# Kernel tuning notes

Measured on AMD Instinct MI355X. Metric: run time of the kernel, lower is better.

The kernel has to match this reference:

```python
import jax, jax.numpy as jnp
import numpy as np

F_IN, F_OUT, N_HEADS = 64, 256, 4
HEAD_DIM = F_OUT // N_HEADS


def setup_inputs() -> dict:
    key = jax.random.key(0)
    ks = jax.random.split(key, 9)
    s_in = 1.0 / np.sqrt(F_IN)
    s_out = 1.0 / np.sqrt(F_OUT)
    return {
        "x": jax.random.normal(ks[0], (4, 32, F_IN, 512), dtype=jnp.float32),
        "Wq": jax.random.normal(ks[1], (F_IN, F_OUT), dtype=jnp.float32) * s_in,
        "bq": jax.random.normal(ks[2], (F_OUT,), dtype=jnp.float32) * 0.01,
        "Wk": jax.random.normal(ks[3], (F_IN, F_OUT), dtype=jnp.float32) * s_in,
        "bk": jax.random.normal(ks[4], (F_OUT,), dtype=jnp.float32) * 0.01,
        "Wv": jax.random.normal(ks[5], (F_IN, F_OUT), dtype=jnp.float32) * s_in,
        "bv": jax.random.normal(ks[6], (F_OUT,), dtype=jnp.float32) * 0.01,
        "Wo": jax.random.normal(ks[7], (F_OUT, F_OUT), dtype=jnp.float32) * s_out,
        "bo": jax.random.normal(ks[8], (F_OUT,), dtype=jnp.float32) * 0.01,
    }


def reference(x, Wq, bq, Wk, bk, Wv, bv, Wo, bo):
    B, N, Fdim, T = x.shape
    xp = jnp.transpose(x, (0, 1, 3, 2))  # [B, N, T, F]
    q = xp @ Wq + bq  # [B, N, T, f_out]
    k = xp @ Wk + bk
    v = xp @ Wv + bv
    # split f_out into heads: [B, N, T, H, hd]
    q = q.reshape(B, N, T, N_HEADS, HEAD_DIM)
    k = k.reshape(B, N, T, N_HEADS, HEAD_DIM)
    v = v.reshape(B, N, T, N_HEADS, HEAD_DIM)
    scale = 1.0 / np.sqrt(HEAD_DIM)
    # full TxT score matrix per (batch, node, head), as in the original
    scores = jnp.einsum("bnqhd,bnkhd->bnhqk", q, k) * scale
    attn = jax.nn.softmax(scores, axis=-1)
    out = jnp.einsum("bnhqk,bnkhd->bnqhd", attn, v)  # [B, N, T, H, hd]
    out = out.reshape(B, N, T, F_OUT)  # head-concat along feature dim
    out = out @ Wo + bo  # fc_out; dropout is identity at inference
    return jnp.transpose(out, (0, 1, 3, 2))  # [B, N, f_out, T]
```

## Files before the change

kernel.cpp:

```cpp
#include <hip/hip_runtime.h>

constexpr int kT = 512;
constexpr int kF = 64;
constexpr int kC = 256;
constexpr int kH = 4;
constexpr int kHD = 64;
constexpr int kBN = 128;

typedef __attribute__((ext_vector_type(4))) float f32x4;
typedef __attribute__((ext_vector_type(8))) short s16x8;
typedef __attribute__((ext_vector_type(4))) unsigned int u32x4;

__device__ inline unsigned short f2bf(float f) {
  unsigned int u = __float_as_uint(f);
  u += 0x7fff + ((u >> 16) & 1);
  return (unsigned short)(u >> 16);
}

__device__ inline float max3f(float a, float b, float c) {
  return fmaxf(fmaxf(a, b), c);
}

__device__ inline float exp2_hw(float x) {
  float r;
  asm("v_exp_f32 %0, %1" : "=v"(r) : "v"(x));
  return r;
}

__global__ __launch_bounds__(256) void k_prep(
    const float* __restrict__ Wq, const float* __restrict__ Wk,
    const float* __restrict__ Wv, const float* __restrict__ Wo,
    unsigned short* __restrict__ WB, unsigned short* __restrict__ WoT) {
  int i = blockIdx.x * 256 + threadIdx.x;
  const int total = 768 * 64 + 256 * 256;
  for (; i < total; i += gridDim.x * 256) {
    if (i < 768 * 64) {
      int c = i >> 6, f = i & 63;
      int arr = c >> 8, cc = c & 255;
      const float* W = (arr == 0) ? Wq : (arr == 1) ? Wk : Wv;
      WB[i] = f2bf(W[f * 256 + cc]);
    } else {
      int j = i - 768 * 64;
      int co = j >> 8, c = j & 255;
      WoT[j] = f2bf(Wo[c * 256 + co]);
    }
  }
}

__global__ __launch_bounds__(1024, 4) void k_fattn(
    const float* __restrict__ x, const unsigned short* __restrict__ WB,
    const float* __restrict__ bq, const float* __restrict__ bk,
    const float* __restrict__ bv, unsigned short* __restrict__ Aw) {
  __shared__ __align__(16) unsigned char smem[149504];
  unsigned char* Kl = smem;
  unsigned char* VtB = smem + 65536;
  unsigned short* xC = (unsigned short*)(smem + 131072);

  const int tid = threadIdx.x;
  const int lbn = blockIdx.x >> 2;
  const int h = blockIdx.x & 3;
  const int lane = tid & 63, wid = tid >> 6;
  const int lr = lane & 15, lg = lane >> 4;
  const int swz = (lr & 7) << 4;

  const float kQscale = 0.180336880111120426f;
  const unsigned short* WBq = WB + (size_t)(h * 64) * 64;
  const unsigned short* WBk = WB + (size_t)(256 + h * 64) * 64;
  const unsigned short* WBv = WB + (size_t)(512 + h * 64) * 64;

  s16x8 qf[2][2];

  for (int tch = 0; tch < 4; ++tch) {
    __syncthreads();
    const float* xb = x + (size_t)lbn * kF * kT + tch * 128;
#pragma unroll
    for (int it = 0; it < 2; ++it) {
      int idx = tid + it * 1024;
      int f = idx >> 5, t4 = idx & 31;
      float4 v = *(const float4*)(xb + f * kT + t4 * 4);
      xC[(t4 * 4 + 0) * 72 + f] = f2bf(v.x);
      xC[(t4 * 4 + 1) * 72 + f] = f2bf(v.y);
      xC[(t4 * 4 + 2) * 72 + f] = f2bf(v.z);
      xC[(t4 * 4 + 3) * 72 + f] = f2bf(v.w);
    }
    __syncthreads();

#pragma unroll
    for (int j = 0; j < 4; ++j) {
      const int tau = wid * 4 + j;
      const int isV = tau >> 5;
      const int tl = tau & 31;
      const int ct = tl >> 3, tt = tl & 7;
      const unsigned short* Wsrc = isV ? WBv : WBk;
      s16x8 af0 = *(const s16x8*)(Wsrc + (ct * 16 + lr) * 64 + lg * 8);
      s16x8 af1 = *(const s16x8*)(Wsrc + (ct * 16 + lr) * 64 + 32 + lg * 8);
      s16x8 bf0 = *(const s16x8*)&xC[(tt * 16 + lr) * 72 + lg * 8];
      s16x8 bf1 = *(const s16x8*)&xC[(tt * 16 + lr) * 72 + 32 + lg * 8];
      if (!isV) {
        f32x4 a = {0.f, 0.f, 0.f, 0.f};
        a = __builtin_amdgcn_mfma_f32_16x16x32_bf16(af0, bf0, a, 0, 0, 0);
        a = __builtin_amdgcn_mfma_f32_16x16x32_bf16(af1, bf1, a, 0, 0, 0);
        const int dbase = ct * 16 + lg * 4;
        const int t = tch * 128 + tt * 16 + lr;
        float v0 = a[0] + bk[h * 64 + dbase + 0];
        float v1 = a[1] + bk[h * 64 + dbase + 1];
        float v2 = a[2] + bk[h * 64 + dbase + 2];
        float v3 = a[3] + bk[h * 64 + dbase + 3];
        unsigned long long pk =
            (unsigned long long)f2bf(v0) |
            ((unsigned long long)f2bf(v1) << 16) |
            ((unsigned long long)f2bf(v2) << 32) |
            ((unsigned long long)f2bf(v3) << 48);
        *(unsigned long long*)(Kl + ((t * 128 + dbase * 2) ^ ((t & 7) << 4))) = pk;
      } else {
        f32x4 a = {0.f, 0.f, 0.f, 0.f};
        a = __builtin_amdgcn_mfma_f32_16x16x32_bf16(bf0, af0, a, 0, 0, 0);
        a = __builtin_amdgcn_mfma_f32_16x16x32_bf16(bf1, af1, a, 0, 0, 0);
        const int d = ct * 16 + lr;
        const float bias = bv[h * 64 + d];
        const int t0 = tch * 128 + tt * 16 + lg * 4;
        const int pos0 = ((t0 >> 5) << 5) | (((t0 >> 2) & 3) << 3) |
                         (((t0 >> 4) & 1) << 2);
        unsigned long long pk =
            (unsigned long long)f2bf(a[0] + bias) |
            ((unsigned long long)f2bf(a[1] + bias) << 16) |
            ((unsigned long long)f2bf(a[2] + bias) << 32) |
            ((unsigned long long)f2bf(a[3] + bias) << 48);
        *(unsigned long long*)(VtB + ((d * 1024 + pos0 * 2) ^ ((d & 7) << 4))) = pk;
      }
    }

    if ((wid >> 2) == tch) {
      f32x4 qa[2][4];
#pragma unroll
      for (int qt = 0; qt < 2; ++qt) {
        const int ttq = (wid & 3) * 2 + qt;
#pragma unroll
        for (int ct = 0; ct < 4; ++ct) {
          s16x8 af0 = *(const s16x8*)(WBq + (ct * 16 + lr) * 64 + lg * 8);
          s16x8 af1 = *(const s16x8*)(WBq + (ct * 16 + lr) * 64 + 32 + lg * 8);
          s16x8 bf0 = *(const s16x8*)&xC[(ttq * 16 + lr) * 72 + lg * 8];
          s16x8 bf1 = *(const s16x8*)&xC[(ttq * 16 + lr) * 72 + 32 + lg * 8];
          f32x4 a = {0.f, 0.f, 0.f, 0.f};
          a = __builtin_amdgcn_mfma_f32_16x16x32_bf16(af0, bf0, a, 0, 0, 0);
          a = __builtin_amdgcn_mfma_f32_16x16x32_bf16(af1, bf1, a, 0, 0, 0);
          const int dbase = ct * 16 + lg * 4;
#pragma unroll
          for (int r = 0; r < 4; ++r)
            a[r] = (a[r] + bq[h * 64 + dbase + r]) * kQscale;
          qa[qt][ct] = a;
        }
      }
      const int sel = lg >> 1;
#pragma unroll
      for (int qt = 0; qt < 2; ++qt)
#pragma unroll
        for (int half = 0; half < 2; ++half) {
          unsigned int w[4];
#pragma unroll
          for (int i2 = 0; i2 < 4; ++i2) {
            const int r0 = (i2 & 1) * 2;
            const int lgp = (lg & 1) * 2 + (i2 >> 1);
            const int src = lgp * 16 + lr;
            float loA = __shfl(qa[qt][half * 2 + 0][r0], src);
            float hiA = __shfl(qa[qt][half * 2 + 1][r0], src);
            float loB = __shfl(qa[qt][half * 2 + 0][r0 + 1], src);
            float hiB = __shfl(qa[qt][half * 2 + 1][r0 + 1], src);
            float eA = sel ? hiA : loA;
            float eB = sel ? hiB : loB;
            asm("v_cvt_pk_bf16_f32 %0, %1, %2"
                : "=v"(w[i2]) : "v"(eA), "v"(eB));
          }
          qf[qt][half] =
              __builtin_bit_cast(s16x8, (u32x4){w[0], w[1], w[2], w[3]});
        }
    }
  }
  __syncthreads();

  unsigned short* Ab = Aw + (size_t)lbn * kT * kC + h * kHD;
  const int qbase = wid * 32;

  f32x4 o0[4] = {{0,0,0,0},{0,0,0,0},{0,0,0,0},{0,0,0,0}};
  f32x4 o1[4] = {{0,0,0,0},{0,0,0,0},{0,0,0,0},{0,0,0,0}};
  float m0 = -3e38f, m1 = -3e38f, l0 = 0.f, l1 = 0.f;

  const int koff = (lg * 16) ^ swz;
  const unsigned char* kp0 = Kl + lr * 128 + koff;
  const unsigned char* kp1 = Kl + lr * 128 + (koff ^ 64);
  const unsigned char* vp0 = VtB + lr * 1024 + ((lg * 16) ^ swz);
  const unsigned char* vp1 = VtB + lr * 1024 + (((lg * 16) ^ 64) ^ swz);

  unsigned int w0[8], w1[8];

#define SOFTMAX_QT(sa, m, l, o, w)                                            \
  {                                                                           \
    float g0 = max3f(sa[0][0], sa[0][1], sa[0][2]);                           \
    float g1 = max3f(sa[0][3], sa[1][0], sa[1][1]);                           \
    float g2 = max3f(sa[1][2], sa[1][3], sa[2][0]);                           \
    float g3 = max3f(sa[2][1], sa[2][2], sa[2][3]);                           \
    float g4 = max3f(sa[3][0], sa[3][1], sa[3][2]);                           \
    float tm = fmaxf(max3f(g0, g1, g2), max3f(g3, g4, sa[3][3]));             \
    if (__any(tm > m + 8.0f)) {                                               \
      tm = fmaxf(tm, __shfl_xor(tm, 16));                                     \
      tm = fmaxf(tm, __shfl_xor(tm, 32));                                     \
      float mn = fmaxf(m, tm);                                                \
      float al = exp2_hw(m - mn);                                             \
      m = mn;                                                                 \
      l *= al;                                                                \
      float aq0 = __shfl(al, (lane & 48) | (lg * 4 + 0));                     \
      float aq1 = __shfl(al, (lane & 48) | (lg * 4 + 1));                     \
      float aq2 = __shfl(al, (lane & 48) | (lg * 4 + 2));                     \
      float aq3 = __shfl(al, (lane & 48) | (lg * 4 + 3));                     \
      _Pragma("unroll")                                                       \
      for (int dt = 0; dt < 4; ++dt) {                                        \
        o[dt][0] *= aq0; o[dt][1] *= aq1;                                     \
        o[dt][2] *= aq2; o[dt][3] *= aq3;                                     \
      }                                                                       \
    }                                                                         \
    _Pragma("unroll")                                                         \
    for (int s = 0; s < 4; ++s) {                                             \
      float e0 = exp2_hw(sa[s][0] - m);                                       \
      float e1 = exp2_hw(sa[s][1] - m);                                       \
      float e2 = exp2_hw(sa[s][2] - m);                                       \
      float e3 = exp2_hw(sa[s][3] - m);                                       \
      l += (e0 + e1) + (e2 + e3);                                             \
      asm("v_cvt_pk_bf16_f32 %0, %1, %2" : "=v"(w[2*s]) : "v"(e0), "v"(e1));  \
      asm("v_cvt_pk_bf16_f32 %0, %1, %2" : "=v"(w[2*s+1]) : "v"(e2), "v"(e3));\
    }                                                                         \
  }

  for (int kc = 0; kc < 8; ++kc) {
    f32x4 sa0[4], sa1[4];
#pragma unroll
    for (int s = 0; s < 4; ++s) {
      s16x8 kf0 = *(const s16x8*)(kp0 + s * 2048);
      s16x8 kf1 = *(const s16x8*)(kp1 + s * 2048);
      f32x4 z0 = {0.f, 0.f, 0.f, 0.f};
      z0 = __builtin_amdgcn_mfma_f32_16x16x32_bf16(kf0, qf[0][0], z0, 0, 0, 0);
      z0 = __builtin_amdgcn_mfma_f32_16x16x32_bf16(kf1, qf[0][1], z0, 0, 0, 0);
      sa0[s] = z0;
      f32x4 z1 = {0.f, 0.f, 0.f, 0.f};
      z1 = __builtin_amdgcn_mfma_f32_16x16x32_bf16(kf0, qf[1][0], z1, 0, 0, 0);
      z1 = __builtin_amdgcn_mfma_f32_16x16x32_bf16(kf1, qf[1][1], z1, 0, 0, 0);
      sa1[s] = z1;
    }
    kp0 += 8192;
    kp1 += 8192;

    SOFTMAX_QT(sa0, m0, l0, o0, w0)
    SOFTMAX_QT(sa1, m1, l1, o1, w1)

    s16x8 pa00 = __builtin_bit_cast(s16x8, (u32x4){w0[0], w0[1], w0[2], w0[3]});
    s16x8 pa01 = __builtin_bit_cast(s16x8, (u32x4){w0[4], w0[5], w0[6], w0[7]});
    s16x8 pa10 = __builtin_bit_cast(s16x8, (u32x4){w1[0], w1[1], w1[2], w1[3]});
    s16x8 pa11 = __builtin_bit_cast(s16x8, (u32x4){w1[4], w1[5], w1[6], w1[7]});

#pragma unroll
    for (int dt = 0; dt < 4; ++dt) {
      s16x8 vb = *(const s16x8*)(vp0 + dt * 16384);
      o0[dt] = __builtin_amdgcn_mfma_f32_16x16x32_bf16(pa00, vb, o0[dt], 0, 0, 0);
      o1[dt] = __builtin_amdgcn_mfma_f32_16x16x32_bf16(pa10, vb, o1[dt], 0, 0, 0);
    }
#pragma unroll
    for (int dt = 0; dt < 4; ++dt) {
      s16x8 vb = *(const s16x8*)(vp1 + dt * 16384);
      o0[dt] = __builtin_amdgcn_mfma_f32_16x16x32_bf16(pa01, vb, o0[dt], 0, 0, 0);
      o1[dt] = __builtin_amdgcn_mfma_f32_16x16x32_bf16(pa11, vb, o1[dt], 0, 0, 0);
    }
    vp0 += 128;
    vp1 += 128;
  }
#undef SOFTMAX_QT

#pragma unroll
  for (int qt = 0; qt < 2; ++qt) {
    float l = (qt == 0) ? l0 : l1;
    f32x4* o = (qt == 0) ? o0 : o1;
    float l2 = l + __shfl_xor(l, 16);
    float lr4 = l2 + __shfl_xor(l2, 32);
    float li0 = 1.0f / __shfl(lr4, (lane & 48) | (lg * 4 + 0));
    float li1 = 1.0f / __shfl(lr4, (lane & 48) | (lg * 4 + 1));
    float li2 = 1.0f / __shfl(lr4, (lane & 48) | (lg * 4 + 2));
    float li3 = 1.0f / __shfl(lr4, (lane & 48) | (lg * 4 + 3));
    const int qb = qbase + qt * 16;
#pragma unroll
    for (int r = 0; r < 4; ++r) {
      float li = (r == 0) ? li0 : (r == 1) ? li1 : (r == 2) ? li2 : li3;
      unsigned short* orow = Ab + (size_t)(qb + lg * 4 + r) * kC;
#pragma unroll
      for (int dt = 0; dt < 4; ++dt)
        orow[dt * 16 + lr] = f2bf(o[dt][r] * li);
    }
  }
}

__global__ __launch_bounds__(512) void k_proj(
    const unsigned short* __restrict__ Aw, const unsigned short* __restrict__ WoT,
    const float* __restrict__ bo, float* __restrict__ out) {
  __shared__ __align__(16) unsigned char Al[128 * 512];

  const int tid = threadIdx.x;
  const int lbn = blockIdx.x >> 2;
  const int tch = blockIdx.x & 3;
  const int t0 = tch * 128;

  const uint4* Asrc = (const uint4*)(Aw + ((size_t)lbn * kT + t0) * kC);
#pragma unroll
  for (int i = 0; i < 8; ++i) {
    int idx = tid + i * 512;
    int trow = idx >> 5, cc = idx & 31;
    *(uint4*)(Al + ((trow * 512 + cc * 16) ^ ((trow & 7) << 4))) = Asrc[idx];
  }
  __syncthreads();

  const int lane = tid & 63, wid = tid >> 6;
  const int lr = lane & 15, lg = lane >> 4;
  const int swz = (lr & 7) << 4;
  const int tb = (wid >> 2) * 64;
  const int cob = (wid & 3) * 64;

  float* ob = out + (size_t)lbn * kC * kT;

  for (int ci = 0; ci < 4; ++ci) {
    const int co0 = cob + ci * 16;
    s16x8 af[8];
#pragma unroll
    for (int kc = 0; kc < 8; ++kc)
      af[kc] = *(const s16x8*)(WoT + (size_t)(co0 + lr) * 256 + kc * 32 + lg * 8);
    float b4[4];
#pragma unroll
    for (int r = 0; r < 4; ++r) b4[r] = bo[co0 + lg * 4 + r];

#pragma unroll
    for (int tj = 0; tj < 4; ++tj) {
      const unsigned char* ap = Al + (tb + tj * 16 + lr) * 512;
      f32x4 acc = {0.f, 0.f, 0.f, 0.f};
#pragma unroll
      for (int kc = 0; kc < 8; ++kc) {
        s16x8 bfr = *(const s16x8*)(ap + ((kc * 64 + lg * 16) ^ swz));
        acc = __builtin_amdgcn_mfma_f32_16x16x32_bf16(af[kc], bfr, acc, 0, 0, 0);
      }
      int t = t0 + tb + tj * 16 + lr;
#pragma unroll
      for (int r = 0; r < 4; ++r)
        ob[(size_t)(co0 + lg * 4 + r) * kT + t] = acc[r] + b4[r];
    }
  }
}

extern "C" void kernel_launch(void* const* d_in, const int* in_sizes, int n_in,
                              void* d_out, int out_size, void* d_ws, size_t ws_size,
                              hipStream_t stream) {
  const float* x  = (const float*)d_in[0];
  const float* Wq = (const float*)d_in[1];
  const float* bq = (const float*)d_in[2];
  const float* Wk = (const float*)d_in[3];
  const float* bk = (const float*)d_in[4];
  const float* Wv = (const float*)d_in[5];
  const float* bv = (const float*)d_in[6];
  const float* Wo = (const float*)d_in[7];
  const float* bo = (const float*)d_in[8];
  float* out = (float*)d_out;

  const size_t wElems = 768 * 64 + 256 * 256;
  const size_t aBytes = (size_t)kBN * kT * kC * 2;
  if (ws_size < wElems * 2 + aBytes) return;

  unsigned short* WB  = (unsigned short*)d_ws;
  unsigned short* WoT = WB + 768 * 64;
  unsigned short* A   = WB + wElems;

  k_prep<<<dim3(448), dim3(256), 0, stream>>>(Wq, Wk, Wv, Wo, WB, WoT);
  k_fattn<<<dim3(kBN * kH), dim3(1024), 0, stream>>>(x, WB, bq, bk, bv, A);
  k_proj<<<dim3(kBN * 4), dim3(512), 0, stream>>>(A, WoT, bo, out);
}
```

Before: 118.4 us.

## Swizzle x staging tile, remap block order, prefetch V fragments, use packed bf16 converts

The x staging buffer in LDS gets an XOR swizzle (144-byte rows) in place of the padded 72-element layout, to cut bank conflicts on fragment reads. Block IDs are remapped so consecutive blocks spread across node/head groups, which changes how work lands on XCDs and caches. V fragments are loaded before the softmax so LDS latency overlaps the exp work. Manual bf16 rounding is replaced with the hardware v_cvt_pk_bf16_f32 instruction throughout. The early V loads raise register pressure in a 1024-thread block, and the block remap may hurt L2 locality of x reuse.

Result: no change. 120.7 us (+1.9%).

```diff
diff --git a/kernel.cpp b/kernel.cpp
--- a/kernel.cpp
+++ b/kernel.cpp
@@ -15,6 +15,12 @@
   unsigned int u = __float_as_uint(f);
   u += 0x7fff + ((u >> 16) & 1);
   return (unsigned short)(u >> 16);
+}
+
+__device__ inline unsigned int cvt_pk(float a, float b) {
+  unsigned int w;
+  asm("v_cvt_pk_bf16_f32 %0, %1, %2" : "=v"(w) : "v"(a), "v"(b));
+  return w;
 }
 
 __device__ inline float max3f(float a, float b, float c) {
@@ -54,11 +60,13 @@
   __shared__ __align__(16) unsigned char smem[149504];
   unsigned char* Kl = smem;
   unsigned char* VtB = smem + 65536;
-  unsigned short* xC = (unsigned short*)(smem + 131072);
+  unsigned char* xCb = smem + 131072;
 
   const int tid = threadIdx.x;
-  const int lbn = blockIdx.x >> 2;
-  const int h = blockIdx.x & 3;
+  const int bid = blockIdx.x;
+  const int orig = (bid & 7) * 64 + (bid >> 3);
+  const int lbn = orig >> 2;
+  const int h = orig & 3;
   const int lane = tid & 63, wid = tid >> 6;
   const int lr = lane & 15, lg = lane >> 4;
   const int swz = (lr & 7) << 4;
@@ -68,6 +76,9 @@
   const unsigned short* WBk = WB + (size_t)(256 + h * 64) * 64;
   const unsigned short* WBv = WB + (size_t)(512 + h * 64) * 64;
 
+#define XFRAG(r, c) (const s16x8*)(xCb + (r) * 144 + \
+    (((c) * 2) ^ ((((r) >> 2) & 7) << 4)))
+
   s16x8 qf[2][2];
 
   for (int tch = 0; tch < 4; ++tch) {
@@ -78,10 +89,15 @@
       int idx = tid + it * 1024;
       int f = idx >> 5, t4 = idx & 31;
       float4 v = *(const float4*)(xb + f * kT + t4 * 4);
-      xC[(t4 * 4 + 0) * 72 + f] = f2bf(v.x);
-      xC[(t4 * 4 + 1) * 72 + f] = f2bf(v.y);
-      xC[(t4 * 4 + 2) * 72 + f] = f2bf(v.z);
-      xC[(t4 * 4 + 3) * 72 + f] = f2bf(v.w);
+      unsigned int wlo = cvt_pk(v.x, v.y);
+      unsigned int whi = cvt_pk(v.z, v.w);
+      const int fb = f * 2;
+      const int colb = (fb & 15) | ((((fb >> 4) ^ (t4 & 7))) << 4);
+      unsigned char* rp = xCb + (t4 * 4) * 144 + colb;
+      *(unsigned short*)(rp + 0 * 144) = (unsigned short)wlo;
+      *(unsigned short*)(rp + 1 * 144) = (unsigned short)(wlo >> 16);
+      *(unsigned short*)(rp + 2 * 144) = (unsigned short)whi;
+      *(unsigned short*)(rp + 3 * 144) = (unsigned short)(whi >> 16);
     }
     __syncthreads();
 
@@ -94,24 +110,20 @@
       const unsigned short* Wsrc = isV ? WBv : WBk;
       s16x8 af0 = *(const s16x8*)(Wsrc + (ct * 16 + lr) * 64 + lg * 8);
       s16x8 af1 = *(const s16x8*)(Wsrc + (ct * 16 + lr) * 64 + 32 + lg * 8);
-      s16x8 bf0 = *(const s16x8*)&xC[(tt * 16 + lr) * 72 + lg * 8];
-      s16x8 bf1 = *(const s16x8*)&xC[(tt * 16 + lr) * 72 + 32 + lg * 8];
+      s16x8 bf0 = *XFRAG(tt * 16 + lr, lg * 8);
+      s16x8 bf1 = *XFRAG(tt * 16 + lr, 32 + lg * 8);
       if (!isV) {
         f32x4 a = {0.f, 0.f, 0.f, 0.f};
         a = __builtin_amdgcn_mfma_f32_16x16x32_bf16(af0, bf0, a, 0, 0, 0);
         a = __builtin_amdgcn_mfma_f32_16x16x32_bf16(af1, bf1, a, 0, 0, 0);
         const int dbase = ct * 16 + lg * 4;
         const int t = tch * 128 + tt * 16 + lr;
-        float v0 = a[0] + bk[h * 64 + dbase + 0];
-        float v1 = a[1] + bk[h * 64 + dbase + 1];
-        float v2 = a[2] + bk[h * 64 + dbase + 2];
-        float v3 = a[3] + bk[h * 64 + dbase + 3];
-        unsigned long long pk =
-            (unsigned long long)f2bf(v0) |
-            ((unsigned long long)f2bf(v1) << 16) |
-            ((unsigned long long)f2bf(v2) << 32) |
-            ((unsigned long long)f2bf(v3) << 48);
-        *(unsigned long long*)(Kl + ((t * 128 + dbase * 2) ^ ((t & 7) << 4))) = pk;
+        uint2 pk;
+        pk.x = cvt_pk(a[0] + bk[h * 64 + dbase + 0],
+                      a[1] + bk[h * 64 + dbase + 1]);
+        pk.y = cvt_pk(a[2] + bk[h * 64 + dbase + 2],
+                      a[3] + bk[h * 64 + dbase + 3]);
+        *(uint2*)(Kl + ((t * 128 + dbase * 2) ^ ((t & 7) << 4))) = pk;
       } else {
         f32x4 a = {0.f, 0.f, 0.f, 0.f};
         a = __builtin_amdgcn_mfma_f32_16x16x32_bf16(bf0, af0, a, 0, 0, 0);
@@ -121,12 +133,10 @@
         const int t0 = tch * 128 + tt * 16 + lg * 4;
         const int pos0 = ((t0 >> 5) << 5) | (((t0 >> 2) & 3) << 3) |
                          (((t0 >> 4) & 1) << 2);
-        unsigned long long pk =
-            (unsigned long long)f2bf(a[0] + bias) |
-            ((unsigned long long)f2bf(a[1] + bias) << 16) |
-            ((unsigned long long)f2bf(a[2] + bias) << 32) |
-            ((unsigned long long)f2bf(a[3] + bias) << 48);
-        *(unsigned long long*)(VtB + ((d * 1024 + pos0 * 2) ^ ((d & 7) << 4))) = pk;
+        uint2 pk;
+        pk.x = cvt_pk(a[0] + bias, a[1] + bias);
+        pk.y = cvt_pk(a[2] + bias, a[3] + bias);
+        *(uint2*)(VtB + ((d * 1024 + pos0 * 2) ^ ((d & 7) << 4))) = pk;
       }
     }
 
@@ -139,8 +149,8 @@
         for (int ct = 0; ct < 4; ++ct) {
           s16x8 af0 = *(const s16x8*)(WBq + (ct * 16 + lr) * 64 + lg * 8);
           s16x8 af1 = *(const s16x8*)(WBq + (ct * 16 + lr) * 64 + 32 + lg * 8);
-          s16x8 bf0 = *(const s16x8*)&xC[(ttq * 16 + lr) * 72 + lg * 8];
-          s16x8 bf1 = *(const s16x8*)&xC[(ttq * 16 + lr) * 72 + 32 + lg * 8];
+          s16x8 bf0 = *XFRAG(ttq * 16 + lr, lg * 8);
+          s16x8 bf1 = *XFRAG(ttq * 16 + lr, 32 + lg * 8);
           f32x4 a = {0.f, 0.f, 0.f, 0.f};
           a = __builtin_amdgcn_mfma_f32_16x16x32_bf16(af0, bf0, a, 0, 0, 0);
           a = __builtin_amdgcn_mfma_f32_16x16x32_bf16(af1, bf1, a, 0, 0, 0);
@@ -166,10 +176,7 @@
             float hiA = __shfl(qa[qt][half * 2 + 1][r0], src);
             float loB = __shfl(qa[qt][half * 2 + 0][r0 + 1], src);
             float hiB = __shfl(qa[qt][half * 2 + 1][r0 + 1], src);
-            float eA = sel ? hiA : loA;
-            float eB = sel ? hiB : loB;
-            asm("v_cvt_pk_bf16_f32 %0, %1, %2"
-                : "=v"(w[i2]) : "v"(eA), "v"(eB));
+            w[i2] = cvt_pk(sel ? hiA : loA, sel ? hiB : loB);
           }
           qf[qt][half] =
               __builtin_bit_cast(s16x8, (u32x4){w[0], w[1], w[2], w[3]});
@@ -177,6 +184,7 @@
     }
   }
   __syncthreads();
+#undef XFRAG
 
   unsigned short* Ab = Aw + (size_t)lbn * kT * kC + h * kHD;
   const int qbase = wid * 32;
@@ -225,8 +233,8 @@
       float e2 = exp2_hw(sa[s][2] - m);                                       \
       float e3 = exp2_hw(sa[s][3] - m);                                       \
       l += (e0 + e1) + (e2 + e3);                                             \
-      asm("v_cvt_pk_bf16_f32 %0, %1, %2" : "=v"(w[2*s]) : "v"(e0), "v"(e1));  \
-      asm("v_cvt_pk_bf16_f32 %0, %1, %2" : "=v"(w[2*s+1]) : "v"(e2), "v"(e3));\
+      w[2*s]   = cvt_pk(e0, e1);                                              \
+      w[2*s+1] = cvt_pk(e2, e3);                                              \
     }                                                                         \
   }
 
@@ -248,6 +256,15 @@
     kp0 += 8192;
     kp1 += 8192;
 
+    s16x8 vb0[4], vb1[4];
+#pragma unroll
+    for (int dt = 0; dt < 4; ++dt) {
+      vb0[dt] = *(const s16x8*)(vp0 + dt * 16384);
+      vb1[dt] = *(const s16x8*)(vp1 + dt * 16384);
+    }
+    vp0 += 128;
+    vp1 += 128;
+
     SOFTMAX_QT(sa0, m0, l0, o0, w0)
     SOFTMAX_QT(sa1, m1, l1, o1, w1)
 
@@ -258,18 +275,14 @@
 
 #pragma unroll
     for (int dt = 0; dt < 4; ++dt) {
-      s16x8 vb = *(const s16x8*)(vp0 + dt * 16384);
-      o0[dt] = __builtin_amdgcn_mfma_f32_16x16x32_bf16(pa00, vb, o0[dt], 0, 0, 0);
-      o1[dt] = __builtin_amdgcn_mfma_f32_16x16x32_bf16(pa10, vb, o1[dt], 0, 0, 0);
+      o0[dt] = __builtin_amdgcn_mfma_f32_16x16x32_bf16(pa00, vb0[dt], o0[dt], 0, 0, 0);
+      o1[dt] = __builtin_amdgcn_mfma_f32_16x16x32_bf16(pa10, vb0[dt], o1[dt], 0, 0, 0);
     }
 #pragma unroll
     for (int dt = 0; dt < 4; ++dt) {
-      s16x8 vb = *(const s16x8*)(vp1 + dt * 16384);
-      o0[dt] = __builtin_amdgcn_mfma_f32_16x16x32_bf16(pa01, vb, o0[dt], 0, 0, 0);
-      o1[dt] = __builtin_amdgcn_mfma_f32_16x16x32_bf16(pa11, vb, o1[dt], 0, 0, 0);
-    }
-    vp0 += 128;
-    vp1 += 128;
+      o0[dt] = __builtin_amdgcn_mfma_f32_16x16x32_bf16(pa01, vb1[dt], o0[dt], 0, 0, 0);
+      o1[dt] = __builtin_amdgcn_mfma_f32_16x16x32_bf16(pa11, vb1[dt], o1[dt], 0, 0, 0);
+    }
   }
 #undef SOFTMAX_QT
 
@@ -288,9 +301,12 @@
     for (int r = 0; r < 4; ++r) {
       float li = (r == 0) ? li0 : (r == 1) ? li1 : (r == 2) ? li2 : li3;
       unsigned short* orow = Ab + (size_t)(qb + lg * 4 + r) * kC;
-#pragma unroll
-      for (int dt = 0; dt < 4; ++dt)
-        orow[dt * 16 + lr] = f2bf(o[dt][r] * li);
+      unsigned int wa = cvt_pk(o[0][r] * li, o[1][r] * li);
+      unsigned int wb = cvt_pk(o[2][r] * li, o[3][r] * li);
+      orow[0 * 16 + lr] = (unsigned short)wa;
+      orow[1 * 16 + lr] = (unsigned short)(wa >> 16);
+      orow[2 * 16 + lr] = (unsigned short)wb;
+      orow[3 * 16 + lr] = (unsigned short)(wb >> 16);
     }
   }
 }
```
